# Optimization experiments

Measured on AMD Instinct MI355X. Metric: run time of the kernel, lower is better.

Reference implementation:

```python
import jax, jax.numpy as jnp
import numpy as np

# tinygemm asymmetric int4 convention
QUANT_MIN, QUANT_MAX = 0, 15
MID_POINT = (QUANT_MAX + QUANT_MIN + 1) / 2.0  # 8.0
OUT_F, IN_F, GROUP = 8192, 8192, 128
M_TOKENS = 64


def setup_inputs() -> dict:
    key = jax.random.key(0)
    kx, kw = jax.random.split(key)
    x = jax.random.normal(kx, (M_TOKENS, IN_F), dtype=jnp.float32)
    # Materialize quantized params exactly as quantize_weight_tinygemm does.
    w = jax.random.normal(kw, (OUT_F, IN_F), dtype=jnp.float32) * 0.02
    ng = IN_F // GROUP
    wg = w.reshape(OUT_F, ng, GROUP)
    min_val = wg.min(axis=2)
    max_val = wg.max(axis=2)
    scale = jnp.maximum((max_val - min_val) / float(QUANT_MAX - QUANT_MIN), 1.1920929e-7)
    zero_point = min_val + scale * MID_POINT
    min_val_recon = zero_point - scale * MID_POINT
    q = jnp.clip(jnp.round((wg - min_val_recon[..., None]) / scale[..., None]),
                 QUANT_MIN, QUANT_MAX).astype(jnp.int32)
    int_data = q.reshape(OUT_F, IN_F)  # values in [0, 15]
    # tinygemm layout: (n_groups, out_features, 2) with [..., 0]=scale, [..., 1]=zero_point
    scale_and_zero = jnp.stack([scale, zero_point], axis=-1).transpose(1, 0, 2)
    return {"x": x, "int_data": int_data, "scale_and_zero": scale_and_zero}


def reference(x, int_data, scale_and_zero):
    # Dequant: w = (q - MID_POINT) * scale + zero_point, per group of GROUP along in_features.
    ng = IN_F // GROUP
    q = int_data.reshape(OUT_F, ng, GROUP).astype(x.dtype)
    scale = scale_and_zero[..., 0].T[:, :, None]       # (OUT_F, ng, 1)
    zero_point = scale_and_zero[..., 1].T[:, :, None]  # (OUT_F, ng, 1)
    w = ((q - MID_POINT) * scale + zero_point).reshape(OUT_F, IN_F)
    return x @ w.T  # (M, OUT_F)
```

## Files before the change

### kernel.cpp

```cpp
#include <hip/hip_runtime.h>


#define OUT_F 8192
#define IN_F  8192
#define M_TOK 64
#define GROUP 128
#define BN    32
#define KW    4
#define KR    (IN_F / KW)

typedef short short8 __attribute__((ext_vector_type(8)));
typedef float f32x4  __attribute__((ext_vector_type(4)));
typedef int   int4v  __attribute__((ext_vector_type(4)));

__device__ __forceinline__ int pack_bf2(float lo, float hi) {
    unsigned ul = __float_as_uint(lo) + 0x8000u;
    unsigned uh = __float_as_uint(hi) + 0x8000u;
    return (int)((ul >> 16) | (uh & 0xFFFF0000u));
}

__global__ __launch_bounds__(512, 2)
void woq_gemm(const float* __restrict__ x,
              const int*   __restrict__ qw,
              const float* __restrict__ sz,
              float*       __restrict__ outp) {
    __shared__ f32x4 red[6 * 4 * 64];

    const int t    = threadIdx.x;
    const int lane = t & 63;
    const int wv   = t >> 6;
    const int mh   = wv & 1;
    const int kh   = wv >> 1;
    const int n0   = blockIdx.x * BN;

    const int nlo  = lane & 15;
    const int quad = lane >> 4;
    const int kq8  = quad << 3;

    const int n1 = n0 + nlo;
    const int n2 = n1 + 16;
    const int m0 = mh * 32;

    const float* xr0 = x  + (size_t)(m0 + nlo) * IN_F;
    const float* xr1 = xr0 + (size_t)16 * IN_F;
    const int*   qr1 = qw + (size_t)n1 * IN_F;
    const int*   qr2 = qw + (size_t)n2 * IN_F;

    f32x4 acc[2][2];
#pragma unroll
    for (int mi = 0; mi < 2; ++mi)
#pragma unroll
        for (int ni = 0; ni < 2; ++ni)
            acc[mi][ni] = (f32x4){0.f, 0.f, 0.f, 0.f};

    const int kbase = kh * KR;

    for (int g = 0; g < KR / GROUP; ++g) {
        const int kg = kbase + g * GROUP;
        const int gg = kg >> 7;

        const float2 p1 = *(const float2*)(sz + ((size_t)gg * OUT_F + n1) * 2);
        const float2 p2 = *(const float2*)(sz + ((size_t)gg * OUT_F + n2) * 2);
        const float s1 = p1.x, c1 = fmaf(-8.f, p1.x, p1.y);
        const float s2 = p2.x, c2 = fmaf(-8.f, p2.x, p2.y);

#pragma unroll
        for (int ks = 0; ks < 4; ++ks) {
            const int k = kg + ks * 32 + kq8;

            const int4 qa = *(const int4*)(qr1 + k);
            const int4 qb = *(const int4*)(qr1 + k + 4);
            const int4 qc = *(const int4*)(qr2 + k);
            const int4 qd = *(const int4*)(qr2 + k + 4);

            const float4 va0 = *(const float4*)(xr0 + k);
            const float4 va1 = *(const float4*)(xr0 + k + 4);
            const float4 vb0 = *(const float4*)(xr1 + k);
            const float4 vb1 = *(const float4*)(xr1 + k + 4);

            int4v ai0, ai1;
            ai0.x = pack_bf2(va0.x, va0.y);
            ai0.y = pack_bf2(va0.z, va0.w);
            ai0.z = pack_bf2(va1.x, va1.y);
            ai0.w = pack_bf2(va1.z, va1.w);
            ai1.x = pack_bf2(vb0.x, vb0.y);
            ai1.y = pack_bf2(vb0.z, vb0.w);
            ai1.z = pack_bf2(vb1.x, vb1.y);
            ai1.w = pack_bf2(vb1.z, vb1.w);
            const short8 a0 = __builtin_bit_cast(short8, ai0);
            const short8 a1 = __builtin_bit_cast(short8, ai1);

            int4v b1i, b2i;
            b1i.x = pack_bf2(fmaf((float)qa.x, s1, c1), fmaf((float)qa.y, s1, c1));
            b1i.y = pack_bf2(fmaf((float)qa.z, s1, c1), fmaf((float)qa.w, s1, c1));
            b1i.z = pack_bf2(fmaf((float)qb.x, s1, c1), fmaf((float)qb.y, s1, c1));
            b1i.w = pack_bf2(fmaf((float)qb.z, s1, c1), fmaf((float)qb.w, s1, c1));
            b2i.x = pack_bf2(fmaf((float)qc.x, s2, c2), fmaf((float)qc.y, s2, c2));
            b2i.y = pack_bf2(fmaf((float)qc.z, s2, c2), fmaf((float)qc.w, s2, c2));
            b2i.z = pack_bf2(fmaf((float)qd.x, s2, c2), fmaf((float)qd.y, s2, c2));
            b2i.w = pack_bf2(fmaf((float)qd.z, s2, c2), fmaf((float)qd.w, s2, c2));
            const short8 b1 = __builtin_bit_cast(short8, b1i);
            const short8 b2 = __builtin_bit_cast(short8, b2i);

            acc[0][0] = __builtin_amdgcn_mfma_f32_16x16x32_bf16(a0, b1, acc[0][0], 0, 0, 0);
            acc[1][0] = __builtin_amdgcn_mfma_f32_16x16x32_bf16(a1, b1, acc[1][0], 0, 0, 0);
            acc[0][1] = __builtin_amdgcn_mfma_f32_16x16x32_bf16(a0, b2, acc[0][1], 0, 0, 0);
            acc[1][1] = __builtin_amdgcn_mfma_f32_16x16x32_bf16(a1, b2, acc[1][1], 0, 0, 0);
        }
    }

    if (kh > 0) {
        const int sb = ((kh - 1) * 2 + mh) * 4 * 64;
#pragma unroll
        for (int mi = 0; mi < 2; ++mi)
#pragma unroll
            for (int ni = 0; ni < 2; ++ni)
                red[sb + (mi * 2 + ni) * 64 + lane] = acc[mi][ni];
    }
    __syncthreads();
    if (kh == 0) {
#pragma unroll
        for (int p = 0; p < 3; ++p) {
            const int sb = (p * 2 + mh) * 4 * 64;
#pragma unroll
            for (int mi = 0; mi < 2; ++mi)
#pragma unroll
                for (int ni = 0; ni < 2; ++ni)
                    acc[mi][ni] += red[sb + (mi * 2 + ni) * 64 + lane];
        }
#pragma unroll
        for (int mi = 0; mi < 2; ++mi)
#pragma unroll
            for (int ni = 0; ni < 2; ++ni) {
                const int n = n0 + ni * 16 + nlo;
#pragma unroll
                for (int r = 0; r < 4; ++r) {
                    const int m = m0 + mi * 16 + quad * 4 + r;
                    outp[(size_t)m * OUT_F + n] = acc[mi][ni][r];
                }
            }
    }
}

extern "C" void kernel_launch(void* const* d_in, const int* in_sizes, int n_in,
                              void* d_out, int out_size, void* d_ws, size_t ws_size,
                              hipStream_t stream) {
    const float* x  = (const float*)d_in[0];
    const int*   qw = (const int*)d_in[1];
    const float* sz = (const float*)d_in[2];
    float* out = (float*)d_out;

    woq_gemm<<<dim3(OUT_F / BN), 512, 0, stream>>>(x, qw, sz, out);
}
```

Before: 444.7 us.

## Use 16-column tiles with 8-way K split and register-prefetch weight loads

Halves the output tile width to 16 columns, which doubles the block count, and splits K across all 8 waves. Each wave now covers all 64 tokens with four MFMAs that share one dequantized B fragment. Weight loads are software-pipelined two iterations ahead in registers, and bf16 packing switches to the HIP intrinsic. Each block now re-reads x for all 64 rows, and the larger 8-way reduction adds shared-memory traffic.

```diff
diff --git a/kernel.cpp b/kernel.cpp
--- a/kernel.cpp
+++ b/kernel.cpp
@@ -1,36 +1,37 @@
 #include <hip/hip_runtime.h>
+#include <hip/hip_bf16.h>
 
 
 #define OUT_F 8192
 #define IN_F  8192
 #define M_TOK 64
 #define GROUP 128
-#define BN    32
-#define KW    4
-#define KR    (IN_F / KW)
+#define BN    16
+#define KWAVE 8
+#define KR    (IN_F / KWAVE)
+#define ITERS (KR / 32)
 
 typedef short short8 __attribute__((ext_vector_type(8)));
 typedef float f32x4  __attribute__((ext_vector_type(4)));
-typedef int   int4v  __attribute__((ext_vector_type(4)));
+typedef unsigned u32x4 __attribute__((ext_vector_type(4)));
 
-__device__ __forceinline__ int pack_bf2(float lo, float hi) {
-    unsigned ul = __float_as_uint(lo) + 0x8000u;
-    unsigned uh = __float_as_uint(hi) + 0x8000u;
-    return (int)((ul >> 16) | (uh & 0xFFFF0000u));
+__device__ __forceinline__ unsigned pk(float lo, float hi) {
+    __hip_bfloat162 h = __float22bfloat162_rn(float2{lo, hi});
+    unsigned r;
+    __builtin_memcpy(&r, &h, sizeof(r));
+    return r;
 }
 
-__global__ __launch_bounds__(512, 2)
+__global__ __launch_bounds__(512, 4)
 void woq_gemm(const float* __restrict__ x,
               const int*   __restrict__ qw,
               const float* __restrict__ sz,
               float*       __restrict__ outp) {
-    __shared__ f32x4 red[6 * 4 * 64];
+    __shared__ f32x4 red[8 * 4 * 64];
 
     const int t    = threadIdx.x;
     const int lane = t & 63;
     const int wv   = t >> 6;
-    const int mh   = wv & 1;
-    const int kh   = wv >> 1;
     const int n0   = blockIdx.x * BN;
 
     const int nlo  = lane & 15;
@@ -38,107 +39,94 @@
     const int kq8  = quad << 3;
 
     const int n1 = n0 + nlo;
-    const int n2 = n1 + 16;
-    const int m0 = mh * 32;
+    const int*   qr = qw + (size_t)n1 * IN_F;
+    const float* xr = x  + (size_t)nlo * IN_F;
+    const int kbase = wv * KR;
 
-    const float* xr0 = x  + (size_t)(m0 + nlo) * IN_F;
-    const float* xr1 = xr0 + (size_t)16 * IN_F;
-    const int*   qr1 = qw + (size_t)n1 * IN_F;
-    const int*   qr2 = qw + (size_t)n2 * IN_F;
+    f32x4 acc[4];
+#pragma unroll
+    for (int mi = 0; mi < 4; ++mi) acc[mi] = (f32x4){0.f, 0.f, 0.f, 0.f};
 
-    f32x4 acc[2][2];
+    int4 wa0, wb0, wa1, wb1;
+    {
+        const int* p0 = qr + kbase + kq8;
+        wa0 = *(const int4*)(p0);
+        wb0 = *(const int4*)(p0 + 4);
+        const int* p1 = qr + kbase + 32 + kq8;
+        wa1 = *(const int4*)(p1);
+        wb1 = *(const int4*)(p1 + 4);
+    }
+
+    float s1 = 0.f, c1 = 0.f;
+
+#pragma unroll 4
+    for (int it = 0; it < ITERS; ++it) {
+        if ((it & 3) == 0) {
+            const int gg = (kbase + it * 32) >> 7;
+            const float2 p = *(const float2*)(sz + ((size_t)gg * OUT_F + n1) * 2);
+            s1 = p.x;
+            c1 = fmaf(-8.f, p.x, p.y);
+        }
+
+        const int kk = kbase + it * 32;
+
+        float4 xv[4][2];
 #pragma unroll
-    for (int mi = 0; mi < 2; ++mi)
+        for (int mi = 0; mi < 4; ++mi) {
+            const float4* xp = (const float4*)(xr + (size_t)mi * 16 * IN_F + kk + kq8);
+            xv[mi][0] = xp[0];
+            xv[mi][1] = xp[1];
+        }
+
+        int4 wa2, wb2;
+        {
+            const int itn = (it + 2 < ITERS) ? it + 2 : ITERS - 1;
+            const int* pn = qr + kbase + itn * 32 + kq8;
+            wa2 = *(const int4*)(pn);
+            wb2 = *(const int4*)(pn + 4);
+        }
+
+        short8 a[4];
 #pragma unroll
-        for (int ni = 0; ni < 2; ++ni)
-            acc[mi][ni] = (f32x4){0.f, 0.f, 0.f, 0.f};
+        for (int mi = 0; mi < 4; ++mi) {
+            u32x4 ai;
+            ai.x = pk(xv[mi][0].x, xv[mi][0].y);
+            ai.y = pk(xv[mi][0].z, xv[mi][0].w);
+            ai.z = pk(xv[mi][1].x, xv[mi][1].y);
+            ai.w = pk(xv[mi][1].z, xv[mi][1].w);
+            a[mi] = __builtin_bit_cast(short8, ai);
+        }
 
-    const int kbase = kh * KR;
-
-    for (int g = 0; g < KR / GROUP; ++g) {
-        const int kg = kbase + g * GROUP;
-        const int gg = kg >> 7;
-
-        const float2 p1 = *(const float2*)(sz + ((size_t)gg * OUT_F + n1) * 2);
-        const float2 p2 = *(const float2*)(sz + ((size_t)gg * OUT_F + n2) * 2);
-        const float s1 = p1.x, c1 = fmaf(-8.f, p1.x, p1.y);
-        const float s2 = p2.x, c2 = fmaf(-8.f, p2.x, p2.y);
+        u32x4 bi;
+        bi.x = pk(fmaf((float)wa0.x, s1, c1), fmaf((float)wa0.y, s1, c1));
+        bi.y = pk(fmaf((float)wa0.z, s1, c1), fmaf((float)wa0.w, s1, c1));
+        bi.z = pk(fmaf((float)wb0.x, s1, c1), fmaf((float)wb0.y, s1, c1));
+        bi.w = pk(fmaf((float)wb0.z, s1, c1), fmaf((float)wb0.w, s1, c1));
+        const short8 b = __builtin_bit_cast(short8, bi);
 
 #pragma unroll
-        for (int ks = 0; ks < 4; ++ks) {
-            const int k = kg + ks * 32 + kq8;
+        for (int mi = 0; mi < 4; ++mi)
+            acc[mi] = __builtin_amdgcn_mfma_f32_16x16x32_bf16(a[mi], b, acc[mi], 0, 0, 0);
 
-            const int4 qa = *(const int4*)(qr1 + k);
-            const int4 qb = *(const int4*)(qr1 + k + 4);
-            const int4 qc = *(const int4*)(qr2 + k);
-            const int4 qd = *(const int4*)(qr2 + k + 4);
-
-            const float4 va0 = *(const float4*)(xr0 + k);
-            const float4 va1 = *(const float4*)(xr0 + k + 4);
-            const float4 vb0 = *(const float4*)(xr1 + k);
-            const float4 vb1 = *(const float4*)(xr1 + k + 4);
-
-            int4v ai0, ai1;
-            ai0.x = pack_bf2(va0.x, va0.y);
-            ai0.y = pack_bf2(va0.z, va0.w);
-            ai0.z = pack_bf2(va1.x, va1.y);
-            ai0.w = pack_bf2(va1.z, va1.w);
-            ai1.x = pack_bf2(vb0.x, vb0.y);
-            ai1.y = pack_bf2(vb0.z, vb0.w);
-            ai1.z = pack_bf2(vb1.x, vb1.y);
-            ai1.w = pack_bf2(vb1.z, vb1.w);
-            const short8 a0 = __builtin_bit_cast(short8, ai0);
-            const short8 a1 = __builtin_bit_cast(short8, ai1);
-
-            int4v b1i, b2i;
-            b1i.x = pack_bf2(fmaf((float)qa.x, s1, c1), fmaf((float)qa.y, s1, c1));
-            b1i.y = pack_bf2(fmaf((float)qa.z, s1, c1), fmaf((float)qa.w, s1, c1));
-            b1i.z = pack_bf2(fmaf((float)qb.x, s1, c1), fmaf((float)qb.y, s1, c1));
-            b1i.w = pack_bf2(fmaf((float)qb.z, s1, c1), fmaf((float)qb.w, s1, c1));
-            b2i.x = pack_bf2(fmaf((float)qc.x, s2, c2), fmaf((float)qc.y, s2, c2));
-            b2i.y = pack_bf2(fmaf((float)qc.z, s2, c2), fmaf((float)qc.w, s2, c2));
-            b2i.z = pack_bf2(fmaf((float)qd.x, s2, c2), fmaf((float)qd.y, s2, c2));
-            b2i.w = pack_bf2(fmaf((float)qd.z, s2, c2), fmaf((float)qd.w, s2, c2));
-            const short8 b1 = __builtin_bit_cast(short8, b1i);
-            const short8 b2 = __builtin_bit_cast(short8, b2i);
-
-            acc[0][0] = __builtin_amdgcn_mfma_f32_16x16x32_bf16(a0, b1, acc[0][0], 0, 0, 0);
-            acc[1][0] = __builtin_amdgcn_mfma_f32_16x16x32_bf16(a1, b1, acc[1][0], 0, 0, 0);
-            acc[0][1] = __builtin_amdgcn_mfma_f32_16x16x32_bf16(a0, b2, acc[0][1], 0, 0, 0);
-            acc[1][1] = __builtin_amdgcn_mfma_f32_16x16x32_bf16(a1, b2, acc[1][1], 0, 0, 0);
-        }
+        wa0 = wa1; wb0 = wb1;
+        wa1 = wa2; wb1 = wb2;
     }
 
-    if (kh > 0) {
-        const int sb = ((kh - 1) * 2 + mh) * 4 * 64;
 #pragma unroll
-        for (int mi = 0; mi < 2; ++mi)
+    for (int mi = 0; mi < 4; ++mi)
+        red[(wv * 4 + mi) * 64 + lane] = acc[mi];
+    __syncthreads();
+
+    if (wv < 4) {
+        f32x4 s = red[(0 * 4 + wv) * 64 + lane];
 #pragma unroll
-            for (int ni = 0; ni < 2; ++ni)
-                red[sb + (mi * 2 + ni) * 64 + lane] = acc[mi][ni];
-    }
-    __syncthreads();
-    if (kh == 0) {
+        for (int sl = 1; sl < 8; ++sl)
+            s += red[(sl * 4 + wv) * 64 + lane];
 #pragma unroll
-        for (int p = 0; p < 3; ++p) {
-            const int sb = (p * 2 + mh) * 4 * 64;
-#pragma unroll
-            for (int mi = 0; mi < 2; ++mi)
-#pragma unroll
-                for (int ni = 0; ni < 2; ++ni)
-                    acc[mi][ni] += red[sb + (mi * 2 + ni) * 64 + lane];
+        for (int r = 0; r < 4; ++r) {
+            const int m = wv * 16 + quad * 4 + r;
+            outp[(size_t)m * OUT_F + n0 + nlo] = s[r];
         }
-#pragma unroll
-        for (int mi = 0; mi < 2; ++mi)
-#pragma unroll
-            for (int ni = 0; ni < 2; ++ni) {
-                const int n = n0 + ni * 16 + nlo;
-#pragma unroll
-                for (int r = 0; r < 4; ++r) {
-                    const int m = m0 + mi * 16 + quad * 4 + r;
-                    outp[(size_t)m * OUT_F + n] = acc[mi][ni][r];
-                }
-            }
     }
 }
 
@@ -148,7 +136,5 @@
     const float* x  = (const float*)d_in[0];
     const int*   qw = (const int*)d_in[1];
     const float* sz = (const float*)d_in[2];
-    float* out = (float*)d_out;
-
-    woq_gemm<<<dim3(OUT_F / BN), 512, 0, stream>>>(x, qw, sz, out);
+    woq_gemm<<<dim3(OUT_F / BN), 512, 0, stream>>>(x, qw, sz, (float*)d_out);
 }
```

New measurement: 471.2 us. 1.06x slower.
